# Kernel optimization log

Hardware: AMD Instinct MI355X
Metric: run time of the kernel (lower is better)

## Reference

```python
import jax, jax.numpy as jnp
import numpy as np

B, L, K = 8, 1024, 30
NUM_RBF = 16
NPOS = 16
MAXREL = 32
EDGE = 128
EDGE_IN = NPOS + NUM_RBF * 25  # 416

# 25 atom-pair order (ProteinMPNN convention) over atoms [Ca=0, N=1, C=2, O=3, Cb=4]
PAIR_I = np.array([0,1,2,3,4,0,0,0,0,1,1,1,4,4,3,1,2,3,4,2,3,4,2,3,2])
PAIR_J = np.array([0,1,2,3,4,1,2,3,4,2,3,4,2,3,2,0,0,0,0,1,1,1,4,4,3])


def setup_inputs() -> dict:
    key = jax.random.key(0)
    ks = jax.random.split(key, 8)
    X = jax.random.normal(ks[0], (B, L, 4, 3), dtype=jnp.float32) * 3.0
    mask = jnp.ones((B, L), dtype=jnp.float32)
    residue_idx = jnp.arange(B * L, dtype=jnp.int64 if jax.config.jax_enable_x64 else jnp.int32).reshape(B, L)
    S = jax.random.randint(ks[1], (B, L), 0, 21)
    SSE3_seq = jax.random.randint(ks[2], (B, L), 0, 4)
    SSE8_seq = jax.random.randint(ks[3], (B, L), 0, 9)
    W_pos = jax.random.normal(ks[4], (2 * MAXREL + 2, NPOS), dtype=jnp.float32) * 0.02
    b_pos = jnp.zeros((NPOS,), dtype=jnp.float32)
    W_edge = jax.random.normal(ks[5], (EDGE_IN, EDGE), dtype=jnp.float32) * 0.02
    ln_gamma = jnp.ones((EDGE,), dtype=jnp.float32)
    ln_beta = jnp.zeros((EDGE,), dtype=jnp.float32)
    return {"X": X, "mask": mask, "residue_idx": residue_idx, "S": S,
            "SSE3_seq": SSE3_seq, "SSE8_seq": SSE8_seq,
            "W_pos": W_pos, "b_pos": b_pos, "W_edge": W_edge,
            "ln_gamma": ln_gamma, "ln_beta": ln_beta}


def _forward(X, mask, residue_idx, W_pos, b_pos, W_edge, ln_gamma, ln_beta):
    N = X[:, :, 0, :]
    Ca = X[:, :, 1, :]
    C = X[:, :, 2, :]
    O = X[:, :, 3, :]
    b = Ca - N
    c = C - Ca
    a = jnp.cross(b, c)
    Cb = -0.58273431 * a + 0.56802827 * b - 0.54067466 * c + Ca

    # _dist: masked pairwise Ca distances, k smallest
    mask2 = mask[:, :, None] * mask[:, None, :]                      # [B,L,L]
    D = mask2 * jnp.sqrt(jnp.sum((Ca[:, :, None] - Ca[:, None]) ** 2, -1) + 1e-6)
    D_max = jnp.max(D, axis=-1, keepdims=True)
    D_adjust = D + (1.0 - mask2) * D_max
    _, E_idx = jax.lax.top_k(-D_adjust, K)                           # [B,L,K] smallest

    # 25 atom-pair RBFs: gather neighbor atoms, then pairwise atom distances
    atoms = jnp.stack([Ca, N, C, O, Cb], axis=2)                     # [B,L,5,3]
    atoms_nb = jax.vmap(lambda a, i: a[i])(atoms, E_idx)             # [B,L,K,5,3]
    Dp = jnp.sqrt(jnp.sum((atoms[:, :, None, :, None, :] - atoms_nb[:, :, :, None, :, :]) ** 2, -1) + 1e-6)  # [B,L,K,5,5]
    mu = jnp.linspace(2.0, 22.0, NUM_RBF)
    sigma = (22.0 - 2.0) / NUM_RBF
    rbf = jnp.exp(-(((Dp[..., None] - mu) / sigma) ** 2))            # [B,L,K,5,5,R]
    rbf_all = rbf[:, :, :, PAIR_I, PAIR_J, :].reshape(Dp.shape[0], Dp.shape[1], K, 25 * NUM_RBF)

    # positional encodings of relative residue index
    offset = residue_idx[:, :, None] - residue_idx[:, None, :]       # [B,L,L]
    off_nb = jnp.take_along_axis(offset, E_idx, axis=2)              # [B,L,K]
    d = jnp.clip(off_nb + MAXREL, 0, 2 * MAXREL)
    E_pos = W_pos[d] + b_pos                                         # [B,L,K,NPOS]

    E = jnp.concatenate([E_pos, rbf_all], axis=-1) @ W_edge          # [B,L,K,EDGE]
    m = jnp.mean(E, axis=-1, keepdims=True)
    v = jnp.mean((E - m) ** 2, axis=-1, keepdims=True)
    E = (E - m) / jnp.sqrt(v + 1e-5) * ln_gamma + ln_beta
    return E, E_idx


def reference(X, mask, residue_idx, S, SSE3_seq, SSE8_seq, W_pos, b_pos, W_edge, ln_gamma, ln_beta):
    return _forward(X, mask, residue_idx, W_pos, b_pos, W_edge, ln_gamma, ln_beta)
```

## Files before the change

kernel.cpp:

```cpp
#include <hip/hip_runtime.h>

#define BB 8
#define LL 1024
#define KNB 30
#define NUM_RBF 16
#define NPOS 16
#define MAXREL 32
#define EDGE_C 128
#define EDGE_IN 416
#define NKK 26
#define WTF_N (NKK * 4 * 64 * 8)

__constant__ int PAIR_I_d[25] = {0,1,2,3,4,0,0,0,0,1,1,1,4,4,3,1,2,3,4,2,3,4,2,3,2};
__constant__ int PAIR_J_d[25] = {0,1,2,3,4,1,2,3,4,2,3,4,2,3,2,0,0,0,0,1,1,1,4,4,3};

typedef _Float16 half8 __attribute__((ext_vector_type(8)));
typedef float floatx16 __attribute__((ext_vector_type(16)));

__global__ __launch_bounds__(256) void knn_kernel(const float* __restrict__ X,
                                                  const float* __restrict__ mask,
                                                  float* __restrict__ out_idx,
                                                  const float* __restrict__ W_edge,
                                                  _Float16* __restrict__ WtF) {
    if (blockIdx.x >= 2048) {
        int o = (blockIdx.x - 2048) * 256 + threadIdx.x;
        if (o < WTF_N) {
            int j = o & 7, l = (o >> 3) & 63, w = (o >> 9) & 3, kk = o >> 11;
            int k = (kk << 4) + ((l >> 5) << 3) + j;
            int n = (w << 5) + (l & 31);
            WtF[o] = (_Float16)W_edge[k * EDGE_C + n];
        }
        return;
    }

    int b = blockIdx.x >> 8;
    int i0 = (blockIdx.x & 255) * 4;
    int tid = threadIdx.x;
    int lane = tid & 63;
    int wv = tid >> 6;

    __shared__ float sCa[LL * 3];
    __shared__ float sMask[LL];

    for (int j = tid; j < LL; j += 256) {
        int base = (b * LL + j) * 12 + 3;
        sCa[j * 3 + 0] = X[base + 0];
        sCa[j * 3 + 1] = X[base + 1];
        sCa[j * 3 + 2] = X[base + 2];
        sMask[j] = mask[b * LL + j];
    }
    __syncthreads();

    int i = i0 + wv;
    int row = b * LL + i;
    float cax = sCa[i * 3 + 0], cay = sCa[i * 3 + 1], caz = sCa[i * 3 + 2];
    float mi = sMask[i];

    float Dv[16];
    float dmax = 0.0f;
#pragma unroll
    for (int c = 0; c < 16; ++c) {
        int j = lane + c * 64;
        float dx = cax - sCa[j * 3 + 0];
        float dy = cay - sCa[j * 3 + 1];
        float dz = caz - sCa[j * 3 + 2];
        float m2 = mi * sMask[j];
        float D = m2 * sqrtf(dx * dx + dy * dy + dz * dz + 1e-6f);
        Dv[c] = D;
        dmax = fmaxf(dmax, D);
    }
    for (int o = 32; o; o >>= 1) dmax = fmaxf(dmax, __shfl_down(dmax, o));
    dmax = __shfl(dmax, 0);

    double cand[16];
#pragma unroll
    for (int c = 0; c < 16; ++c) {
        int j = lane + c * 64;
        float m2 = mi * sMask[j];
        float Dadj = Dv[c] + (1.0f - m2) * dmax;
        unsigned int bits = __float_as_uint(Dadj);
        cand[c] = fma((double)bits, 1024.0, (double)j);
    }

    const double KILL = 9.0e15;
    float myj = 0.0f;
    for (int r = 0; r < KNB; ++r) {
        double a0 = fmin(cand[0], cand[1]);
        double a1 = fmin(cand[2], cand[3]);
        double a2 = fmin(cand[4], cand[5]);
        double a3 = fmin(cand[6], cand[7]);
        double a4 = fmin(cand[8], cand[9]);
        double a5 = fmin(cand[10], cand[11]);
        double a6 = fmin(cand[12], cand[13]);
        double a7 = fmin(cand[14], cand[15]);
        a0 = fmin(a0, a1); a2 = fmin(a2, a3); a4 = fmin(a4, a5); a6 = fmin(a6, a7);
        a0 = fmin(a0, a2); a4 = fmin(a4, a6);
        double m = fmin(a0, a4);
        for (int o = 32; o; o >>= 1) {
            double other = __shfl_down(m, o);
            m = fmin(m, other);
        }
        m = __shfl(m, 0);
        unsigned long long ku = (unsigned long long)m;
        int jw = __builtin_amdgcn_readfirstlane((int)(ku & 1023));
        bool own = (lane == (jw & 63));
        switch (jw >> 6) {
            case 0:  if (own) cand[0]  = KILL; break;
            case 1:  if (own) cand[1]  = KILL; break;
            case 2:  if (own) cand[2]  = KILL; break;
            case 3:  if (own) cand[3]  = KILL; break;
            case 4:  if (own) cand[4]  = KILL; break;
            case 5:  if (own) cand[5]  = KILL; break;
            case 6:  if (own) cand[6]  = KILL; break;
            case 7:  if (own) cand[7]  = KILL; break;
            case 8:  if (own) cand[8]  = KILL; break;
            case 9:  if (own) cand[9]  = KILL; break;
            case 10: if (own) cand[10] = KILL; break;
            case 11: if (own) cand[11] = KILL; break;
            case 12: if (own) cand[12] = KILL; break;
            case 13: if (own) cand[13] = KILL; break;
            case 14: if (own) cand[14] = KILL; break;
            case 15: if (own) cand[15] = KILL; break;
        }
        if (lane == r) myj = (float)jw;
    }
    if (lane < KNB) out_idx[(size_t)row * KNB + lane] = myj;
}

__global__ __launch_bounds__(256) void edge_kernel(const float* __restrict__ X,
                                                   const int* __restrict__ ridx,
                                                   const float* __restrict__ W_pos,
                                                   const float* __restrict__ b_pos,
                                                   const _Float16* __restrict__ WtF,
                                                   const float* __restrict__ gamma,
                                                   const float* __restrict__ beta,
                                                   const float* __restrict__ out_idx,
                                                   float* __restrict__ out_E) {
    int row = blockIdx.x;
    int b = row >> 10;
    int i = row & 1023;
    int tid = threadIdx.x;

    __shared__ __align__(16) char smem[29872];
    _Float16* fA = (_Float16*)smem;
    float* Esh = (float*)smem;
    float* atoms = (float*)smem;
    float* dist = (float*)(smem + 26624);
    int* nbr = (int*)(smem + 29624);
    int* dclip = (int*)(smem + 29744);

    if (tid < KNB) {
        int jn = (int)out_idx[(size_t)row * KNB + tid];
        nbr[tid] = jn;
        int off = ridx[row] - ridx[b * LL + jn];
        int d = off + MAXREL;
        d = d < 0 ? 0 : (d > 2 * MAXREL ? 2 * MAXREL : d);
        dclip[tid] = d;
    }
    __syncthreads();

    if (tid < 31) {
        int r = (tid == 0) ? i : nbr[tid - 1];
        int base = (b * LL + r) * 12;
        float Nx = X[base + 0], Ny = X[base + 1], Nz = X[base + 2];
        float Cax = X[base + 3], Cay = X[base + 4], Caz = X[base + 5];
        float Cx = X[base + 6], Cy = X[base + 7], Cz = X[base + 8];
        float Ox = X[base + 9], Oy = X[base + 10], Oz = X[base + 11];
        float bx = Cax - Nx, by = Cay - Ny, bz = Caz - Nz;
        float cx = Cx - Cax, cy = Cy - Cay, cz = Cz - Caz;
        float ax = by * cz - bz * cy;
        float ay = bz * cx - bx * cz;
        float az = bx * cy - by * cx;
        float Cbx = -0.58273431f * ax + 0.56802827f * bx - 0.54067466f * cx + Cax;
        float Cby = -0.58273431f * ay + 0.56802827f * by - 0.54067466f * cy + Cay;
        float Cbz = -0.58273431f * az + 0.56802827f * bz - 0.54067466f * cz + Caz;
        float* A = &atoms[tid * 15];
        A[0] = Cax; A[1] = Cay; A[2] = Caz;
        A[3] = Nx;  A[4] = Ny;  A[5] = Nz;
        A[6] = Cx;  A[7] = Cy;  A[8] = Cz;
        A[9] = Ox;  A[10] = Oy; A[11] = Oz;
        A[12] = Cbx; A[13] = Cby; A[14] = Cbz;
    }
    __syncthreads();

    for (int idx = tid; idx < KNB * 25; idx += 256) {
        int k = idx / 25;
        int p = idx - k * 25;
        const float* Ai = &atoms[PAIR_I_d[p] * 3];
        const float* Aj = &atoms[(1 + k) * 15 + PAIR_J_d[p] * 3];
        float dx = Ai[0] - Aj[0], dy = Ai[1] - Aj[1], dz = Ai[2] - Aj[2];
        dist[idx] = sqrtf(dx * dx + dy * dy + dz * dz + 1e-6f);
    }
    __syncthreads();

    {
        int m = tid & 31;
        int kgb = tid >> 5;
#pragma unroll
        for (int r = 0; r < 7; ++r) {
            int kg = kgb + 8 * r;
            if (kg < 52) {
                half8 v8;
                if (m >= KNB) {
#pragma unroll
                    for (int jj = 0; jj < 8; ++jj) v8[jj] = (_Float16)0.0f;
                } else if (kg < 2) {
                    const float* wp = &W_pos[dclip[m] * NPOS + kg * 8];
                    const float* bp = &b_pos[kg * 8];
#pragma unroll
                    for (int jj = 0; jj < 8; ++jj) v8[jj] = (_Float16)(wp[jj] + bp[jj]);
                } else {
                    int q0 = kg * 8 - 16;
                    int p = q0 >> 4;
                    float t = 0.8f * dist[m * 25 + p] - 1.6f - ((q0 & 8) ? 8.5333336f : 0.0f);
#pragma unroll
                    for (int jj = 0; jj < 8; ++jj) {
                        float x = t - 1.0666667f * (float)jj;
                        v8[jj] = (_Float16)__expf(-x * x);
                    }
                }
                int pos = ((kg >> 1) * 64 + m + 32 * (kg & 1)) * 8;
                *(half8*)(fA + pos) = v8;
            }
        }
    }
    __syncthreads();

    int wv = tid >> 6;
    int l = tid & 63;
    floatx16 acc;
#pragma unroll
    for (int r = 0; r < 16; ++r) acc[r] = 0.0f;

    const half8* Ap = (const half8*)fA + l;
    const half8* Bp = (const half8*)WtF + wv * 64 + l;
#pragma unroll 4
    for (int kk = 0; kk < NKK; ++kk) {
        half8 a = Ap[kk * 64];
        half8 bfr = Bp[kk * 256];
        acc = __builtin_amdgcn_mfma_f32_32x32x16_f16(a, bfr, acc, 0, 0, 0);
    }
    __syncthreads();

#pragma unroll
    for (int r = 0; r < 16; ++r) {
        int rr = (r & 3) + 8 * (r >> 2) + 4 * (l >> 5);
        Esh[rr * EDGE_C + wv * 32 + (l & 31)] = acc[r];
    }
    __syncthreads();

    int cg = tid & 31;
    int ky = tid >> 5;
    int c0 = cg * 4;
    float gam[4], bet[4];
#pragma unroll
    for (int c = 0; c < 4; ++c) { gam[c] = gamma[c0 + c]; bet[c] = beta[c0 + c]; }

#pragma unroll
    for (int r2 = 0; r2 < 4; ++r2) {
        int e = ky + 8 * r2;
        float4 v = *(const float4*)&Esh[e * EDGE_C + c0];
        float s = v.x + v.y + v.z + v.w;
        for (int o = 16; o; o >>= 1) s += __shfl_xor(s, o);
        float mean = s * (1.0f / 128.0f);
        float d0 = v.x - mean, d1 = v.y - mean, d2 = v.z - mean, d3 = v.w - mean;
        float vs = d0 * d0 + d1 * d1 + d2 * d2 + d3 * d3;
        for (int o = 16; o; o >>= 1) vs += __shfl_xor(vs, o);
        float inv = 1.0f / sqrtf(vs * (1.0f / 128.0f) + 1e-5f);
        if (e < KNB) {
            float4 o4;
            o4.x = d0 * inv * gam[0] + bet[0];
            o4.y = d1 * inv * gam[1] + bet[1];
            o4.z = d2 * inv * gam[2] + bet[2];
            o4.w = d3 * inv * gam[3] + bet[3];
            *(float4*)(out_E + ((size_t)(row * KNB + e)) * EDGE_C + c0) = o4;
        }
    }
}

extern "C" void kernel_launch(void* const* d_in, const int* in_sizes, int n_in,
                              void* d_out, int out_size, void* d_ws, size_t ws_size,
                              hipStream_t stream) {
    const float* X      = (const float*)d_in[0];
    const float* mask   = (const float*)d_in[1];
    const int*   ridx   = (const int*)d_in[2];
    const float* W_pos  = (const float*)d_in[6];
    const float* b_pos  = (const float*)d_in[7];
    const float* W_edge = (const float*)d_in[8];
    const float* gamma  = (const float*)d_in[9];
    const float* beta   = (const float*)d_in[10];

    float* out_E   = (float*)d_out;
    float* out_idx = out_E + (size_t)BB * LL * KNB * EDGE_C;
    _Float16* WtF  = (_Float16*)d_ws;

    int knn_grid = 2048 + (WTF_N + 255) / 256;
    knn_kernel<<<knn_grid, 256, 0, stream>>>(X, mask, out_idx, W_edge, WtF);
    edge_kernel<<<BB * LL, 256, 0, stream>>>(X, ridx, W_pos, b_pos, WtF,
                                             gamma, beta, out_idx, out_E);
}
```

Measured before the change: 257.2 us.

## Fuse kNN selection and edge featurization into one kernel per 4 rows

The kNN and edge kernels are merged: each block computes top-k for four residues, keeps the neighbor indices and clipped offsets in shared memory, and then runs the RBF/MFMA/LayerNorm edge path for those four rows one after another. The weight conversion moves to its own small kernel. This removes the global round-trip of neighbor indices and one of the large launches. The cost is fewer blocks (2048 instead of 8192), with each block doing the edge work serially for four rows, so there is less parallelism and less latency hiding.

```diff
diff --git a/kernel.cpp b/kernel.cpp
--- a/kernel.cpp
+++ b/kernel.cpp
@@ -17,30 +17,41 @@
 typedef _Float16 half8 __attribute__((ext_vector_type(8)));
 typedef float floatx16 __attribute__((ext_vector_type(16)));
 
-__global__ __launch_bounds__(256) void knn_kernel(const float* __restrict__ X,
-                                                  const float* __restrict__ mask,
-                                                  float* __restrict__ out_idx,
-                                                  const float* __restrict__ W_edge,
-                                                  _Float16* __restrict__ WtF) {
-    if (blockIdx.x >= 2048) {
-        int o = (blockIdx.x - 2048) * 256 + threadIdx.x;
-        if (o < WTF_N) {
-            int j = o & 7, l = (o >> 3) & 63, w = (o >> 9) & 3, kk = o >> 11;
-            int k = (kk << 4) + ((l >> 5) << 3) + j;
-            int n = (w << 5) + (l & 31);
-            WtF[o] = (_Float16)W_edge[k * EDGE_C + n];
-        }
-        return;
-    }
-
+__global__ __launch_bounds__(256) void wprep_kernel(const float* __restrict__ W_edge,
+                                                    _Float16* __restrict__ WtF) {
+    int o = blockIdx.x * 256 + threadIdx.x;
+    if (o >= WTF_N) return;
+    int j = o & 7, l = (o >> 3) & 63, w = (o >> 9) & 3, kk = o >> 11;
+    int k = (kk << 4) + ((l >> 5) << 3) + j;
+    int n = (w << 5) + (l & 31);
+    WtF[o] = (_Float16)W_edge[k * EDGE_C + n];
+}
+
+__global__ __launch_bounds__(256) void fused_kernel(const float* __restrict__ X,
+                                                    const float* __restrict__ mask,
+                                                    const int* __restrict__ ridx,
+                                                    const float* __restrict__ W_pos,
+                                                    const float* __restrict__ b_pos,
+                                                    const _Float16* __restrict__ WtF,
+                                                    const float* __restrict__ gamma,
+                                                    const float* __restrict__ beta,
+                                                    float* __restrict__ out_E,
+                                                    float* __restrict__ out_idx) {
     int b = blockIdx.x >> 8;
     int i0 = (blockIdx.x & 255) * 4;
     int tid = threadIdx.x;
     int lane = tid & 63;
     int wv = tid >> 6;
 
-    __shared__ float sCa[LL * 3];
-    __shared__ float sMask[LL];
+    __shared__ __align__(16) char smem[30584];
+    float* sCa = (float*)smem;
+    float* sMask = (float*)(smem + 12288);
+    _Float16* fA = (_Float16*)smem;
+    float* Esh = (float*)smem;
+    float* atoms = (float*)smem;
+    float* dist = (float*)(smem + 26624);
+    int* nbr4 = (int*)(smem + 29624);
+    int* dclip4 = (int*)(smem + 30104);
 
     for (int j = tid; j < LL; j += 256) {
         int base = (b * LL + j) * 12 + 3;
@@ -51,204 +62,93 @@
     }
     __syncthreads();
 
-    int i = i0 + wv;
-    int row = b * LL + i;
-    float cax = sCa[i * 3 + 0], cay = sCa[i * 3 + 1], caz = sCa[i * 3 + 2];
-    float mi = sMask[i];
-
-    float Dv[16];
-    float dmax = 0.0f;
-#pragma unroll
-    for (int c = 0; c < 16; ++c) {
-        int j = lane + c * 64;
-        float dx = cax - sCa[j * 3 + 0];
-        float dy = cay - sCa[j * 3 + 1];
-        float dz = caz - sCa[j * 3 + 2];
-        float m2 = mi * sMask[j];
-        float D = m2 * sqrtf(dx * dx + dy * dy + dz * dz + 1e-6f);
-        Dv[c] = D;
-        dmax = fmaxf(dmax, D);
+    {
+        int i = i0 + wv;
+        int row = b * LL + i;
+        float cax = sCa[i * 3 + 0], cay = sCa[i * 3 + 1], caz = sCa[i * 3 + 2];
+        float mi = sMask[i];
+
+        float Dv[16];
+        float dmax = 0.0f;
+#pragma unroll
+        for (int c = 0; c < 16; ++c) {
+            int j = lane + c * 64;
+            float dx = cax - sCa[j * 3 + 0];
+            float dy = cay - sCa[j * 3 + 1];
+            float dz = caz - sCa[j * 3 + 2];
+            float m2 = mi * sMask[j];
+            float D = m2 * sqrtf(dx * dx + dy * dy + dz * dz + 1e-6f);
+            Dv[c] = D;
+            dmax = fmaxf(dmax, D);
+        }
+        for (int o = 32; o; o >>= 1) dmax = fmaxf(dmax, __shfl_down(dmax, o));
+        dmax = __shfl(dmax, 0);
+
+        double cand[16];
+#pragma unroll
+        for (int c = 0; c < 16; ++c) {
+            int j = lane + c * 64;
+            float m2 = mi * sMask[j];
+            float Dadj = Dv[c] + (1.0f - m2) * dmax;
+            unsigned int bits = __float_as_uint(Dadj);
+            cand[c] = fma((double)bits, 1024.0, (double)j);
+        }
+
+        const double KILL = 9.0e15;
+        float myj = 0.0f;
+        for (int r = 0; r < KNB; ++r) {
+            double a0 = fmin(cand[0], cand[1]);
+            double a1 = fmin(cand[2], cand[3]);
+            double a2 = fmin(cand[4], cand[5]);
+            double a3 = fmin(cand[6], cand[7]);
+            double a4 = fmin(cand[8], cand[9]);
+            double a5 = fmin(cand[10], cand[11]);
+            double a6 = fmin(cand[12], cand[13]);
+            double a7 = fmin(cand[14], cand[15]);
+            a0 = fmin(a0, a1); a2 = fmin(a2, a3); a4 = fmin(a4, a5); a6 = fmin(a6, a7);
+            a0 = fmin(a0, a2); a4 = fmin(a4, a6);
+            double m = fmin(a0, a4);
+            for (int o = 32; o; o >>= 1) {
+                double other = __shfl_down(m, o);
+                m = fmin(m, other);
+            }
+            m = __shfl(m, 0);
+            unsigned long long ku = (unsigned long long)m;
+            int jw = __builtin_amdgcn_readfirstlane((int)(ku & 1023));
+            bool own = (lane == (jw & 63));
+            switch (jw >> 6) {
+                case 0:  if (own) cand[0]  = KILL; break;
+                case 1:  if (own) cand[1]  = KILL; break;
+                case 2:  if (own) cand[2]  = KILL; break;
+                case 3:  if (own) cand[3]  = KILL; break;
+                case 4:  if (own) cand[4]  = KILL; break;
+                case 5:  if (own) cand[5]  = KILL; break;
+                case 6:  if (own) cand[6]  = KILL; break;
+                case 7:  if (own) cand[7]  = KILL; break;
+                case 8:  if (own) cand[8]  = KILL; break;
+                case 9:  if (own) cand[9]  = KILL; break;
+                case 10: if (own) cand[10] = KILL; break;
+                case 11: if (own) cand[11] = KILL; break;
+                case 12: if (own) cand[12] = KILL; break;
+                case 13: if (own) cand[13] = KILL; break;
+                case 14: if (own) cand[14] = KILL; break;
+                case 15: if (own) cand[15] = KILL; break;
+            }
+            if (lane == r) myj = (float)jw;
+        }
+        if (lane < KNB) {
+            int jn = (int)myj;
+            nbr4[wv * KNB + lane] = jn;
+            int off = ridx[row] - ridx[b * LL + jn];
+            int d = off + MAXREL;
+            d = d < 0 ? 0 : (d > 2 * MAXREL ? 2 * MAXREL : d);
+            dclip4[wv * KNB + lane] = d;
+            out_idx[(size_t)row * KNB + lane] = myj;
+        }
     }
-    for (int o = 32; o; o >>= 1) dmax = fmaxf(dmax, __shfl_down(dmax, o));
-    dmax = __shfl(dmax, 0);
-
-    double cand[16];
-#pragma unroll
-    for (int c = 0; c < 16; ++c) {
-        int j = lane + c * 64;
-        float m2 = mi * sMask[j];
-        float Dadj = Dv[c] + (1.0f - m2) * dmax;
-        unsigned int bits = __float_as_uint(Dadj);
-        cand[c] = fma((double)bits, 1024.0, (double)j);
-    }
-
-    const double KILL = 9.0e15;
-    float myj = 0.0f;
-    for (int r = 0; r < KNB; ++r) {
-        double a0 = fmin(cand[0], cand[1]);
-        double a1 = fmin(cand[2], cand[3]);
-        double a2 = fmin(cand[4], cand[5]);
-        double a3 = fmin(cand[6], cand[7]);
-        double a4 = fmin(cand[8], cand[9]);
-        double a5 = fmin(cand[10], cand[11]);
-        double a6 = fmin(cand[12], cand[13]);
-        double a7 = fmin(cand[14], cand[15]);
-        a0 = fmin(a0, a1); a2 = fmin(a2, a3); a4 = fmin(a4, a5); a6 = fmin(a6, a7);
-        a0 = fmin(a0, a2); a4 = fmin(a4, a6);
-        double m = fmin(a0, a4);
-        for (int o = 32; o; o >>= 1) {
-            double other = __shfl_down(m, o);
-            m = fmin(m, other);
-        }
-        m = __shfl(m, 0);
-        unsigned long long ku = (unsigned long long)m;
-        int jw = __builtin_amdgcn_readfirstlane((int)(ku & 1023));
-        bool own = (lane == (jw & 63));
-        switch (jw >> 6) {
-            case 0:  if (own) cand[0]  = KILL; break;
-            case 1:  if (own) cand[1]  = KILL; break;
-            case 2:  if (own) cand[2]  = KILL; break;
-            case 3:  if (own) cand[3]  = KILL; break;
-            case 4:  if (own) cand[4]  = KILL; break;
-            case 5:  if (own) cand[5]  = KILL; break;
-            case 6:  if (own) cand[6]  = KILL; break;
-            case 7:  if (own) cand[7]  = KILL; break;
-            case 8:  if (own) cand[8]  = KILL; break;
-            case 9:  if (own) cand[9]  = KILL; break;
-            case 10: if (own) cand[10] = KILL; break;
-            case 11: if (own) cand[11] = KILL; break;
-            case 12: if (own) cand[12] = KILL; break;
-            case 13: if (own) cand[13] = KILL; break;
-            case 14: if (own) cand[14] = KILL; break;
-            case 15: if (own) cand[15] = KILL; break;
-        }
-        if (lane == r) myj = (float)jw;
-    }
-    if (lane < KNB) out_idx[(size_t)row * KNB + lane] = myj;
-}
-
-__global__ __launch_bounds__(256) void edge_kernel(const float* __restrict__ X,
-                                                   const int* __restrict__ ridx,
-                                                   const float* __restrict__ W_pos,
-                                                   const float* __restrict__ b_pos,
-                                                   const _Float16* __restrict__ WtF,
-                                                   const float* __restrict__ gamma,
-                                                   const float* __restrict__ beta,
-                                                   const float* __restrict__ out_idx,
-                                                   float* __restrict__ out_E) {
-    int row = blockIdx.x;
-    int b = row >> 10;
-    int i = row & 1023;
-    int tid = threadIdx.x;
-
-    __shared__ __align__(16) char smem[29872];
-    _Float16* fA = (_Float16*)smem;
-    float* Esh = (float*)smem;
-    float* atoms = (float*)smem;
-    float* dist = (float*)(smem + 26624);
-    int* nbr = (int*)(smem + 29624);
-    int* dclip = (int*)(smem + 29744);
-
-    if (tid < KNB) {
-        int jn = (int)out_idx[(size_t)row * KNB + tid];
-        nbr[tid] = jn;
-        int off = ridx[row] - ridx[b * LL + jn];
-        int d = off + MAXREL;
-        d = d < 0 ? 0 : (d > 2 * MAXREL ? 2 * MAXREL : d);
-        dclip[tid] = d;
-    }
-    __syncthreads();
-
-    if (tid < 31) {
-        int r = (tid == 0) ? i : nbr[tid - 1];
-        int base = (b * LL + r) * 12;
-        float Nx = X[base + 0], Ny = X[base + 1], Nz = X[base + 2];
-        float Cax = X[base + 3], Cay = X[base + 4], Caz = X[base + 5];
-        float Cx = X[base + 6], Cy = X[base + 7], Cz = X[base + 8];
-        float Ox = X[base + 9], Oy = X[base + 10], Oz = X[base + 11];
-        float bx = Cax - Nx, by = Cay - Ny, bz = Caz - Nz;
-        float cx = Cx - Cax, cy = Cy - Cay, cz = Cz - Caz;
-        float ax = by * cz - bz * cy;
-        float ay = bz * cx - bx * cz;
-        float az = bx * cy - by * cx;
-        float Cbx = -0.58273431f * ax + 0.56802827f * bx - 0.54067466f * cx + Cax;
-        float Cby = -0.58273431f * ay + 0.56802827f * by - 0.54067466f * cy + Cay;
-        float Cbz = -0.58273431f * az + 0.56802827f * bz - 0.54067466f * cz + Caz;
-        float* A = &atoms[tid * 15];
-        A[0] = Cax; A[1] = Cay; A[2] = Caz;
-        A[3] = Nx;  A[4] = Ny;  A[5] = Nz;
-        A[6] = Cx;  A[7] = Cy;  A[8] = Cz;
-        A[9] = Ox;  A[10] = Oy; A[11] = Oz;
-        A[12] = Cbx; A[13] = Cby; A[14] = Cbz;
-    }
-    __syncthreads();
-
-    for (int idx = tid; idx < KNB * 25; idx += 256) {
-        int k = idx / 25;
-        int p = idx - k * 25;
-        const float* Ai = &atoms[PAIR_I_d[p] * 3];
-        const float* Aj = &atoms[(1 + k) * 15 + PAIR_J_d[p] * 3];
-        float dx = Ai[0] - Aj[0], dy = Ai[1] - Aj[1], dz = Ai[2] - Aj[2];
-        dist[idx] = sqrtf(dx * dx + dy * dy + dz * dz + 1e-6f);
-    }
-    __syncthreads();
-
-    {
-        int m = tid & 31;
-        int kgb = tid >> 5;
-#pragma unroll
-        for (int r = 0; r < 7; ++r) {
-            int kg = kgb + 8 * r;
-            if (kg < 52) {
-                half8 v8;
-                if (m >= KNB) {
-#pragma unroll
-                    for (int jj = 0; jj < 8; ++jj) v8[jj] = (_Float16)0.0f;
-                } else if (kg < 2) {
-                    const float* wp = &W_pos[dclip[m] * NPOS + kg * 8];
-                    const float* bp = &b_pos[kg * 8];
-#pragma unroll
-                    for (int jj = 0; jj < 8; ++jj) v8[jj] = (_Float16)(wp[jj] + bp[jj]);
-                } else {
-                    int q0 = kg * 8 - 16;
-                    int p = q0 >> 4;
-                    float t = 0.8f * dist[m * 25 + p] - 1.6f - ((q0 & 8) ? 8.5333336f : 0.0f);
-#pragma unroll
-                    for (int jj = 0; jj < 8; ++jj) {
-                        float x = t - 1.0666667f * (float)jj;
-                        v8[jj] = (_Float16)__expf(-x * x);
-                    }
-                }
-                int pos = ((kg >> 1) * 64 + m + 32 * (kg & 1)) * 8;
-                *(half8*)(fA + pos) = v8;
-            }
-        }
-    }
-    __syncthreads();
-
-    int wv = tid >> 6;
+
     int l = tid & 63;
-    floatx16 acc;
-#pragma unroll
-    for (int r = 0; r < 16; ++r) acc[r] = 0.0f;
-
-    const half8* Ap = (const half8*)fA + l;
     const half8* Bp = (const half8*)WtF + wv * 64 + l;
-#pragma unroll 4
-    for (int kk = 0; kk < NKK; ++kk) {
-        half8 a = Ap[kk * 64];
-        half8 bfr = Bp[kk * 256];
-        acc = __builtin_amdgcn_mfma_f32_32x32x16_f16(a, bfr, acc, 0, 0, 0);
-    }
-    __syncthreads();
-
-#pragma unroll
-    for (int r = 0; r < 16; ++r) {
-        int rr = (r & 3) + 8 * (r >> 2) + 4 * (l >> 5);
-        Esh[rr * EDGE_C + wv * 32 + (l & 31)] = acc[r];
-    }
-    __syncthreads();
-
     int cg = tid & 31;
     int ky = tid >> 5;
     int c0 = cg * 4;
@@ -256,24 +156,118 @@
 #pragma unroll
     for (int c = 0; c < 4; ++c) { gam[c] = gamma[c0 + c]; bet[c] = beta[c0 + c]; }
 
-#pragma unroll
-    for (int r2 = 0; r2 < 4; ++r2) {
-        int e = ky + 8 * r2;
-        float4 v = *(const float4*)&Esh[e * EDGE_C + c0];
-        float s = v.x + v.y + v.z + v.w;
-        for (int o = 16; o; o >>= 1) s += __shfl_xor(s, o);
-        float mean = s * (1.0f / 128.0f);
-        float d0 = v.x - mean, d1 = v.y - mean, d2 = v.z - mean, d3 = v.w - mean;
-        float vs = d0 * d0 + d1 * d1 + d2 * d2 + d3 * d3;
-        for (int o = 16; o; o >>= 1) vs += __shfl_xor(vs, o);
-        float inv = 1.0f / sqrtf(vs * (1.0f / 128.0f) + 1e-5f);
-        if (e < KNB) {
-            float4 o4;
-            o4.x = d0 * inv * gam[0] + bet[0];
-            o4.y = d1 * inv * gam[1] + bet[1];
-            o4.z = d2 * inv * gam[2] + bet[2];
-            o4.w = d3 * inv * gam[3] + bet[3];
-            *(float4*)(out_E + ((size_t)(row * KNB + e)) * EDGE_C + c0) = o4;
+    for (int r = 0; r < 4; ++r) {
+        int rowr = b * LL + i0 + r;
+        const int* nbr = nbr4 + r * KNB;
+        const int* dclip = dclip4 + r * KNB;
+
+        __syncthreads();
+
+        if (tid < 31) {
+            int rr = (tid == 0) ? (i0 + r) : nbr[tid - 1];
+            int base = (b * LL + rr) * 12;
+            float Nx = X[base + 0], Ny = X[base + 1], Nz = X[base + 2];
+            float Cax = X[base + 3], Cay = X[base + 4], Caz = X[base + 5];
+            float Cx = X[base + 6], Cy = X[base + 7], Cz = X[base + 8];
+            float Ox = X[base + 9], Oy = X[base + 10], Oz = X[base + 11];
+            float bx = Cax - Nx, by = Cay - Ny, bz = Caz - Nz;
+            float cx = Cx - Cax, cy = Cy - Cay, cz = Cz - Caz;
+            float ax = by * cz - bz * cy;
+            float ay = bz * cx - bx * cz;
+            float az = bx * cy - by * cx;
+            float Cbx = -0.58273431f * ax + 0.56802827f * bx - 0.54067466f * cx + Cax;
+            float Cby = -0.58273431f * ay + 0.56802827f * by - 0.54067466f * cy + Cay;
+            float Cbz = -0.58273431f * az + 0.56802827f * bz - 0.54067466f * cz + Caz;
+            float* A = &atoms[tid * 15];
+            A[0] = Cax; A[1] = Cay; A[2] = Caz;
+            A[3] = Nx;  A[4] = Ny;  A[5] = Nz;
+            A[6] = Cx;  A[7] = Cy;  A[8] = Cz;
+            A[9] = Ox;  A[10] = Oy; A[11] = Oz;
+            A[12] = Cbx; A[13] = Cby; A[14] = Cbz;
+        }
+        __syncthreads();
+
+        for (int idx = tid; idx < KNB * 25; idx += 256) {
+            int k = idx / 25;
+            int p = idx - k * 25;
+            const float* Ai = &atoms[PAIR_I_d[p] * 3];
+            const float* Aj = &atoms[(1 + k) * 15 + PAIR_J_d[p] * 3];
+            float dx = Ai[0] - Aj[0], dy = Ai[1] - Aj[1], dz = Ai[2] - Aj[2];
+            dist[idx] = sqrtf(dx * dx + dy * dy + dz * dz + 1e-6f);
+        }
+        __syncthreads();
+
+        {
+            int m = tid & 31;
+            int kgb = tid >> 5;
+#pragma unroll
+            for (int rr = 0; rr < 7; ++rr) {
+                int kg = kgb + 8 * rr;
+                if (kg < 52) {
+                    half8 v8;
+                    if (m >= KNB) {
+#pragma unroll
+                        for (int jj = 0; jj < 8; ++jj) v8[jj] = (_Float16)0.0f;
+                    } else if (kg < 2) {
+                        const float* wp = &W_pos[dclip[m] * NPOS + kg * 8];
+                        const float* bp = &b_pos[kg * 8];
+#pragma unroll
+                        for (int jj = 0; jj < 8; ++jj) v8[jj] = (_Float16)(wp[jj] + bp[jj]);
+                    } else {
+                        int q0 = kg * 8 - 16;
+                        int p = q0 >> 4;
+                        float t = 0.8f * dist[m * 25 + p] - 1.6f - ((q0 & 8) ? 8.5333336f : 0.0f);
+#pragma unroll
+                        for (int jj = 0; jj < 8; ++jj) {
+                            float x = t - 1.0666667f * (float)jj;
+                            v8[jj] = (_Float16)__expf(-x * x);
+                        }
+                    }
+                    int pos = ((kg >> 1) * 64 + m + 32 * (kg & 1)) * 8;
+                    *(half8*)(fA + pos) = v8;
+                }
+            }
+        }
+        __syncthreads();
+
+        floatx16 acc;
+#pragma unroll
+        for (int q = 0; q < 16; ++q) acc[q] = 0.0f;
+        const half8* Ap = (const half8*)fA + l;
+#pragma unroll 4
+        for (int kk = 0; kk < NKK; ++kk) {
+            half8 a = Ap[kk * 64];
+            half8 bfr = Bp[kk * 256];
+            acc = __builtin_amdgcn_mfma_f32_32x32x16_f16(a, bfr, acc, 0, 0, 0);
+        }
+        __syncthreads();
+
+#pragma unroll
+        for (int q = 0; q < 16; ++q) {
+            int rr = (q & 3) + 8 * (q >> 2) + 4 * (l >> 5);
+            Esh[rr * EDGE_C + wv * 32 + (l & 31)] = acc[q];
+        }
+        __syncthreads();
+
+#pragma unroll
+        for (int r2 = 0; r2 < 4; ++r2) {
+            int e = ky + 8 * r2;
+            float4 v = *(const float4*)&Esh[e * EDGE_C + c0];
+            float s = v.x + v.y + v.z + v.w;
+            for (int o = 16; o; o >>= 1) s += __shfl_xor(s, o);
+            float mean = s * (1.0f / 128.0f);
+            float d0 = v.x - mean, d1 = v.y - mean, d2 = v.z - mean, d3 = v.w - mean;
+            float vs = d0 * d0 + d1 * d1 + d2 * d2 + d3 * d3;
+            for (int o = 16; o; o >>= 1) vs += __shfl_xor(vs, o);
+            float inv = 1.0f / sqrtf(vs * (1.0f / 128.0f) + 1e-5f);
+            if (e < KNB) {
+                float4 o4;
+                o4.x = d0 * inv * gam[0] + bet[0];
+                o4.y = d1 * inv * gam[1] + bet[1];
+                o4.z = d2 * inv * gam[2] + bet[2];
+                o4.w = d3 * inv * gam[3] + bet[3];
+                *(float4*)(out_E + ((size_t)(rowr * KNB + e)) * EDGE_C + c0) = o4;
+            }
         }
     }
 }
@@ -294,8 +288,7 @@
     float* out_idx = out_E + (size_t)BB * LL * KNB * EDGE_C;
     _Float16* WtF  = (_Float16*)d_ws;
 
-    int knn_grid = 2048 + (WTF_N + 255) / 256;
-    knn_kernel<<<knn_grid, 256, 0, stream>>>(X, mask, out_idx, W_edge, WtF);
-    edge_kernel<<<BB * LL, 256, 0, stream>>>(X, ridx, W_pos, b_pos, WtF,
-                                             gamma, beta, out_idx, out_E);
+    wprep_kernel<<<(WTF_N + 255) / 256, 256, 0, stream>>>(W_edge, WtF);
+    fused_kernel<<<BB * LL / 4, 256, 0, stream>>>(X, mask, ridx, W_pos, b_pos, WtF,
+                                                  gamma, beta, out_E, out_idx);
 }
```

New measurement: 320.0 us. +24.4%, slower.
